# Performance work log

Measured on AMD Instinct MI355X. Metric: run time of the kernel, lower is better.

The kernel has to match this reference:

```python
import jax, jax.numpy as jnp
import numpy as np

B, S_BERT, L_WORD, D = 64, 512, 256, 768
REDUC, HID, TAGS, POL = 400, 100, 5, 4


def _make_positions():
    # Each word spans 1-2 consecutive subwords; 256 words * max 2 <= 512 subwords.
    rng = np.random.default_rng(0)
    lens = rng.integers(1, 3, size=(B, L_WORD))          # [B, L] in {1,2}
    starts = np.cumsum(lens, axis=1) - lens              # exclusive prefix sum
    ends = starts + lens - 1                             # inclusive end, <= 511
    return jnp.asarray(np.stack([starts, ends], axis=-1), dtype=jnp.int32)


def setup_inputs() -> dict:
    key = jax.random.key(0)
    ks = jax.random.split(key, 8)
    s = 0.02
    return {
        "bert_vectors": jax.random.normal(ks[0], (B, S_BERT, D), jnp.float32),
        "positions": _make_positions(),
        "W_reduc": jax.random.normal(ks[1], (D, REDUC), jnp.float32) * s,
        "b_reduc": jnp.zeros((REDUC,), jnp.float32),
        "W_ap": jax.random.normal(ks[2], (REDUC, HID), jnp.float32) * s,
        "b_ap": jnp.zeros((HID,), jnp.float32),
        "W_op": jax.random.normal(ks[3], (REDUC, HID), jnp.float32) * s,
        "b_op": jnp.zeros((HID,), jnp.float32),
        "W_ap_tag": jax.random.normal(ks[4], (HID, TAGS), jnp.float32) * s,
        "b_ap_tag": jnp.zeros((TAGS,), jnp.float32),
        "W_op_tag": jax.random.normal(ks[5], (HID, TAGS), jnp.float32) * s,
        "b_op_tag": jnp.zeros((TAGS,), jnp.float32),
        # Biaffine: bias=(True, False) -> in1 gets a ones column: [HID+1, POL*HID]
        "W_bi": jax.random.normal(ks[6], (HID + 1, POL * HID), jnp.float32) * s,
    }


def _segment_mean(vectors, positions):
    # vectors: [B, S, D]; positions: [B, L, 2] inclusive (start, end) spans.
    cs = jnp.cumsum(vectors, axis=1)
    cs = jnp.concatenate([jnp.zeros_like(cs[:, :1]), cs], axis=1)   # [B, S+1, D]
    starts = positions[..., 0]
    ends = positions[..., 1]
    hi = jnp.take_along_axis(cs, (ends + 1)[..., None], axis=1)     # [B, L, D]
    lo = jnp.take_along_axis(cs, starts[..., None], axis=1)
    lens = (ends - starts + 1).astype(vectors.dtype)[..., None]
    return (hi - lo) / lens                                          # [B, L, D]


def reference(bert_vectors, positions, W_reduc, b_reduc, W_ap, b_ap, W_op, b_op,
              W_ap_tag, b_ap_tag, W_op_tag, b_op_tag, W_bi):
    pooled = _segment_mean(bert_vectors, positions)                  # [B, L, D]
    h = jax.nn.relu(pooled @ W_reduc + b_reduc)                      # [B, L, 400]
    ap = jax.nn.relu(h @ W_ap + b_ap)                                # [B, L, 100]
    op = jax.nn.relu(h @ W_op + b_op)                                # [B, L, 100]
    ap_out = ap @ W_ap_tag + b_ap_tag                                # [B, L, T]
    op_out = op @ W_op_tag + b_op_tag                                # [B, L, T]
    # Biaffine with bias=(True, False)
    ones = jnp.ones_like(ap[..., :1])
    a1 = jnp.concatenate([ap, ones], axis=-1)                        # [B, L, 101]
    affine = (a1 @ W_bi).reshape(ap.shape[0], ap.shape[1], POL, HID) # [B, L1, P, H]
    triplet = jnp.einsum('biph,bjh->bjip', affine, op)               # [B, L2, L1, P]
    return ap_out, op_out, triplet
```

## Files before the change

### kernel.cpp

```cpp
#include <hip/hip_runtime.h>
#include <hip/hip_bf16.h>

#define B_    64
#define S_    512
#define L_    256
#define D_    768
#define RED_  400
#define REDP_ 512
#define KEFF_ 416
#define HID_  100
#define HIDP_ 128
#define TAGS_ 5
#define POL_  4
#define NBI_  512
#define NAO_  256
#define BL_   (B_ * L_)

typedef __attribute__((ext_vector_type(8))) short short8;
typedef __attribute__((ext_vector_type(4))) float f32x4;
typedef __attribute__((ext_vector_type(4))) unsigned short u16x4;

#define GLOAD_LDS16(gp, lp) __builtin_amdgcn_global_load_lds( \
    (const __attribute__((address_space(1))) void*)(gp),      \
    (__attribute__((address_space(3))) void*)(lp), 16, 0, 0)

__device__ inline float bf2f(unsigned short u) {
    union { unsigned int i; float f; } c; c.i = ((unsigned)u) << 16; return c.f;
}
__device__ inline unsigned short f2bf(float f) {
    __hip_bfloat16 h = __float2bfloat16(f);
    unsigned short u;
    __builtin_memcpy(&u, &h, 2);
    return u;
}

#define SZ0 393216
#define SZ1 131072
#define SZ2 65536
#define SZ3 512
#define SZ4 256
#define PREP_TOT (SZ0 + SZ1 + SZ2 + SZ3 + SZ4)
#define SEG_BLOCKS (BL_ / 4)
#define PREP_BLOCKS ((PREP_TOT + 255) / 256)

__global__ __launch_bounds__(256) void front_kernel(
    const float* __restrict__ bert, const int* __restrict__ pos,
    unsigned short* __restrict__ pooled,
    const float* __restrict__ W_reduc, const float* __restrict__ b_reduc,
    const float* __restrict__ W_ap, const float* __restrict__ b_ap,
    const float* __restrict__ W_op, const float* __restrict__ b_op,
    const float* __restrict__ W_bi,
    unsigned short* __restrict__ WtR, unsigned short* __restrict__ WtAO,
    unsigned short* __restrict__ WtBi,
    float* __restrict__ bR, float* __restrict__ bAO, float* __restrict__ bBi)
{
    if (blockIdx.x < SEG_BLOCKS) {
        int r  = threadIdx.x >> 6;
        int l  = threadIdx.x & 63;
        int bl = blockIdx.x * 4 + r;
        int b  = bl >> 8;
        int s  = pos[bl * 2 + 0];
        int e  = pos[bl * 2 + 1];
        int len = e - s + 1;
        const float* v0 = bert + ((size_t)b * S_ + s) * D_;
        float inv = (len == 2) ? 0.5f : 1.0f;
        unsigned short* outp = pooled + (size_t)bl * D_;
        #pragma unroll
        for (int c = 0; c < 3; ++c) {
            int d = l * 4 + c * 256;
            f32x4 x = *(const f32x4*)(v0 + d);
            if (len == 2) {
                f32x4 y = *(const f32x4*)(v0 + D_ + d);
                x += y;
            }
            u16x4 o;
            #pragma unroll
            for (int j = 0; j < 4; ++j) o[j] = f2bf(x[j] * inv);
            *(u16x4*)(outp + d) = o;
        }
        return;
    }

    int idx = (blockIdx.x - SEG_BLOCKS) * 256 + threadIdx.x;
    if (idx < SZ0) {
        int n = idx / D_, k = idx - n * D_;
        float v = (n < RED_) ? W_reduc[(size_t)k * RED_ + n] : 0.f;
        WtR[idx] = f2bf(v);
    } else if (idx < SZ0 + SZ1) {
        int i = idx - SZ0;
        int n = i >> 9, k = i & 511;
        float v = 0.f;
        if (k < RED_) {
            if (n < HID_)                      v = W_ap[(size_t)k * HID_ + n];
            else if (n >= 128 && n < 128+HID_) v = W_op[(size_t)k * HID_ + (n-128)];
        }
        WtAO[i] = f2bf(v);
    } else if (idx < SZ0 + SZ1 + SZ2) {
        int i = idx - SZ0 - SZ1;
        int n = i >> 7, k = i & 127;
        int p = n >> 7, h = n & 127;
        float v = (h < HID_ && k < HID_) ? W_bi[(size_t)k * RED_ + p * HID_ + h] : 0.f;
        WtBi[i] = f2bf(v);
        if (k == 0) bBi[n] = (h < HID_) ? W_bi[(size_t)HID_ * RED_ + p * HID_ + h] : 0.f;
    } else if (idx < SZ0 + SZ1 + SZ2 + SZ3) {
        int n = idx - SZ0 - SZ1 - SZ2;
        bR[n] = (n < RED_) ? b_reduc[n] : 0.f;
    } else if (idx < PREP_TOT) {
        int n = idx - SZ0 - SZ1 - SZ2 - SZ3;
        bAO[n] = (n < 128) ? ((n < HID_) ? b_ap[n] : 0.f)
                           : (((n-128) < HID_) ? b_op[n-128] : 0.f);
    }
}

__global__ __launch_bounds__(256) void gemm1_kernel(
    const short* __restrict__ A, const short* __restrict__ Bt,
    const float* __restrict__ bias, unsigned short* __restrict__ Co,
    int M, int N, int K)
{
    __shared__ __align__(16) short lds[2][8192];

    const int t  = threadIdx.x;
    const int wv = t >> 6;
    const int ln = t & 63;
    const int wm = wv >> 1;
    const int wn = wv & 1;
    const int bm = blockIdx.x * 128;
    const int bn = blockIdx.y * 128;

    const int srow = t >> 2;
    const int skc  = (t & 3) * 8;

    f32x4 acc[4][4] = {};
    const int NT = K >> 5;

    {
        #pragma unroll
        for (int q = 0; q < 2; ++q) {
            const short* g = A + (size_t)(bm + q * 64 + srow) * K + skc;
            GLOAD_LDS16(g, &lds[0][q * 2048 + wv * 512]);
        }
        #pragma unroll
        for (int q = 0; q < 2; ++q) {
            const short* g = Bt + (size_t)(bn + q * 64 + srow) * K + skc;
            GLOAD_LDS16(g, &lds[0][4096 + q * 2048 + wv * 512]);
        }
    }
    __syncthreads();

    int cur = 0;
    const int lr = ln & 15;
    const int lk = (ln >> 4) * 8;

    for (int kt = 0; kt < NT; ++kt) {
        if (kt + 1 < NT) {
            int k0 = (kt + 1) << 5;
            #pragma unroll
            for (int q = 0; q < 2; ++q) {
                const short* g = A + (size_t)(bm + q * 64 + srow) * K + k0 + skc;
                GLOAD_LDS16(g, &lds[cur ^ 1][q * 2048 + wv * 512]);
            }
            #pragma unroll
            for (int q = 0; q < 2; ++q) {
                const short* g = Bt + (size_t)(bn + q * 64 + srow) * K + k0 + skc;
                GLOAD_LDS16(g, &lds[cur ^ 1][4096 + q * 2048 + wv * 512]);
            }
        }

        const short* As = &lds[cur][0];
        const short* Bs = &lds[cur][4096];
        short8 a[4], b[4];
        #pragma unroll
        for (int fi = 0; fi < 4; ++fi)
            a[fi] = *(const short8*)(As + (wm * 64 + fi * 16 + lr) * 32 + lk);
        #pragma unroll
        for (int fj = 0; fj < 4; ++fj)
            b[fj] = *(const short8*)(Bs + (wn * 64 + fj * 16 + lr) * 32 + lk);
        #pragma unroll
        for (int fi = 0; fi < 4; ++fi)
            #pragma unroll
            for (int fj = 0; fj < 4; ++fj)
                acc[fi][fj] = __builtin_amdgcn_mfma_f32_16x16x32_bf16(
                    a[fi], b[fj], acc[fi][fj], 0, 0, 0);

        __syncthreads();
        cur ^= 1;
    }

    const int row0 = bm + wm * 64 + (ln >> 4) * 4;
    const int col0 = bn + wn * 64 + lr;
    #pragma unroll
    for (int fi = 0; fi < 4; ++fi)
        #pragma unroll
        for (int r = 0; r < 4; ++r) {
            int row = row0 + fi * 16 + r;
            #pragma unroll
            for (int fj = 0; fj < 4; ++fj) {
                int col = col0 + fj * 16;
                float v = fmaxf(acc[fi][fj][r] + bias[col], 0.f);
                Co[(size_t)row * N + col] = f2bf(v);
            }
        }
}

__global__ __launch_bounds__(256) void gemm23_tag_kernel(
    const short* __restrict__ A, const short* __restrict__ Bt,
    const float* __restrict__ bias,
    unsigned short* __restrict__ apOut, unsigned short* __restrict__ opOut,
    const float* __restrict__ Wap_tag, const float* __restrict__ bap_tag,
    const float* __restrict__ Wop_tag, const float* __restrict__ bop_tag,
    float* __restrict__ out_tag)
{
    __shared__ __align__(16) short lds[2][8192];
    __shared__ float tagf[128 * 101];
    __shared__ float Wtag[HID_ * TAGS_];
    __shared__ float Btag[TAGS_];

    const int t  = threadIdx.x;
    const int wv = t >> 6;
    const int ln = t & 63;
    const int wm = wv >> 1;
    const int wn = wv & 1;
    const int bm = blockIdx.x * 128;
    const int bn = blockIdx.y * 128;
    const int half = blockIdx.y;

    const float* Wt = half ? Wop_tag : Wap_tag;
    const float* bt = half ? bop_tag : bap_tag;
    for (int i = t; i < HID_ * TAGS_; i += 256) Wtag[i] = Wt[i];
    if (t < TAGS_) Btag[t] = bt[t];

    const int srow = t >> 2;
    const int skc  = (t & 3) * 8;
    const int NT = KEFF_ >> 5;

    f32x4 acc[4][4] = {};

    {
        #pragma unroll
        for (int q = 0; q < 2; ++q) {
            const short* g = A + (size_t)(bm + q * 64 + srow) * REDP_ + skc;
            GLOAD_LDS16(g, &lds[0][q * 2048 + wv * 512]);
        }
        #pragma unroll
        for (int q = 0; q < 2; ++q) {
            const short* g = Bt + (size_t)(bn + q * 64 + srow) * REDP_ + skc;
            GLOAD_LDS16(g, &lds[0][4096 + q * 2048 + wv * 512]);
        }
    }
    __syncthreads();

    int cur = 0;
    const int lr = ln & 15;
    const int lk = (ln >> 4) * 8;

    for (int kt = 0; kt < NT; ++kt) {
        if (kt + 1 < NT) {
            int k0 = (kt + 1) << 5;
            #pragma unroll
            for (int q = 0; q < 2; ++q) {
                const short* g = A + (size_t)(bm + q * 64 + srow) * REDP_ + k0 + skc;
                GLOAD_LDS16(g, &lds[cur ^ 1][q * 2048 + wv * 512]);
            }
            #pragma unroll
            for (int q = 0; q < 2; ++q) {
                const short* g = Bt + (size_t)(bn + q * 64 + srow) * REDP_ + k0 + skc;
                GLOAD_LDS16(g, &lds[cur ^ 1][4096 + q * 2048 + wv * 512]);
            }
        }

        const short* As = &lds[cur][0];
        const short* Bs = &lds[cur][4096];
        short8 a[4], b[4];
        #pragma unroll
        for (int fi = 0; fi < 4; ++fi)
            a[fi] = *(const short8*)(As + (wm * 64 + fi * 16 + lr) * 32 + lk);
        #pragma unroll
        for (int fj = 0; fj < 4; ++fj)
            b[fj] = *(const short8*)(Bs + (wn * 64 + fj * 16 + lr) * 32 + lk);
        #pragma unroll
        for (int fi = 0; fi < 4; ++fi)
            #pragma unroll
            for (int fj = 0; fj < 4; ++fj)
                acc[fi][fj] = __builtin_amdgcn_mfma_f32_16x16x32_bf16(
                    a[fi], b[fj], acc[fi][fj], 0, 0, 0);

        __syncthreads();
        cur ^= 1;
    }

    unsigned short* Co = half ? opOut : apOut;
    const int rl0 = wm * 64 + (ln >> 4) * 4;
    const int cl0 = wn * 64 + lr;
    #pragma unroll
    for (int fi = 0; fi < 4; ++fi)
        #pragma unroll
        for (int r = 0; r < 4; ++r) {
            int rl = rl0 + fi * 16 + r;
            #pragma unroll
            for (int fj = 0; fj < 4; ++fj) {
                int cl = cl0 + fj * 16;
                float v = fmaxf(acc[fi][fj][r] + bias[bn + cl], 0.f);
                Co[(size_t)(bm + rl) * 128 + cl] = f2bf(v);
                if (cl < 101) tagf[rl * 101 + cl] = v;
            }
        }
    __syncthreads();

    if (t < 128) {
        float s[TAGS_];
        #pragma unroll
        for (int g = 0; g < TAGS_; ++g) s[g] = Btag[g];
        const float* rowp = &tagf[t * 101];
        for (int k = 0; k < HID_; ++k) {
            float x = rowp[k];
            #pragma unroll
            for (int g = 0; g < TAGS_; ++g) s[g] += x * Wtag[k * TAGS_ + g];
        }
        float* o = out_tag + (size_t)half * (BL_ * TAGS_) + (size_t)(bm + t) * TAGS_;
        #pragma unroll
        for (int g = 0; g < TAGS_; ++g) o[g] = s[g];
    }
}

__global__ __launch_bounds__(256) void affine_kernel(
    const short* __restrict__ ap, const short* __restrict__ WtBi,
    const float* __restrict__ bBi, unsigned short* __restrict__ affine)
{
    __shared__ __align__(16) short As[16384];
    __shared__ __align__(16) short Bs[16384];

    const int t  = threadIdx.x;
    const int wv = t >> 6;
    const int ln = t & 63;
    const int wm = wv >> 1;
    const int wn = wv & 1;
    const int bm = blockIdx.x * 128;
    const int bn = blockIdx.y * 128;

    const int rsub = ln >> 2;
    const int j8   = (ln & 3) * 8;

    #pragma unroll
    for (int i = 0; i < 8; ++i) {
        int ks = i >> 1, hf = i & 1;
        int rloc = wv * 32 + hf * 16;
        const short* gA = ap + (size_t)(bm + rloc + rsub) * HIDP_ + ks * 32 + j8;
        GLOAD_LDS16(gA, &As[ks * 4096 + rloc * 32]);
        const short* gB = WtBi + (size_t)(bn + rloc + rsub) * HIDP_ + ks * 32 + j8;
        GLOAD_LDS16(gB, &Bs[ks * 4096 + rloc * 32]);
    }
    __syncthreads();

    const int lr = ln & 15;
    const int lk = (ln >> 4) * 8;
    f32x4 acc[4][4] = {};

    #pragma unroll
    for (int ks = 0; ks < 4; ++ks) {
        short8 a[4], b[4];
        #pragma unroll
        for (int fi = 0; fi < 4; ++fi)
            a[fi] = *(const short8*)(As + ks * 4096 + (wm * 64 + fi * 16 + lr) * 32 + lk);
        #pragma unroll
        for (int fj = 0; fj < 4; ++fj)
            b[fj] = *(const short8*)(Bs + ks * 4096 + (wn * 64 + fj * 16 + lr) * 32 + lk);
        #pragma unroll
        for (int fi = 0; fi < 4; ++fi)
            #pragma unroll
            for (int fj = 0; fj < 4; ++fj)
                acc[fi][fj] = __builtin_amdgcn_mfma_f32_16x16x32_bf16(
                    a[fi], b[fj], acc[fi][fj], 0, 0, 0);
    }

    const int row0 = bm + wm * 64 + (ln >> 4) * 4;
    const int col0 = bn + wn * 64 + lr;
    #pragma unroll
    for (int fi = 0; fi < 4; ++fi)
        #pragma unroll
        for (int r = 0; r < 4; ++r) {
            int row = row0 + fi * 16 + r;
            #pragma unroll
            for (int fj = 0; fj < 4; ++fj) {
                int col = col0 + fj * 16;
                affine[(size_t)row * NBI_ + col] = f2bf(acc[fi][fj][r] + bBi[col]);
            }
        }
}

__global__ __launch_bounds__(256) void triplet_kernel(
    const short* __restrict__ op, const short* __restrict__ affine,
    float* __restrict__ out)
{
    __shared__ __align__(16) short As[16384];
    __shared__ __align__(16) short Bs[16384];

    const int t  = threadIdx.x;
    const int wv = t >> 6;
    const int ln = t & 63;
    const int wm = wv >> 1;
    const int wn = wv & 1;
    const int bm = blockIdx.x * 128;
    const int bn = blockIdx.y * 128;
    const int b  = blockIdx.z;

    const short* Ab = op     + (size_t)b * 256 * HIDP_;
    const short* Bb = affine + (size_t)b * 256 * NBI_;

    const int rsub = ln >> 2;
    const int j8   = (ln & 3) * 8;

    #pragma unroll
    for (int i = 0; i < 8; ++i) {
        int ks = i >> 1, hf = i & 1;
        int rloc = wv * 32 + hf * 16;
        const short* gA = Ab + (size_t)(bm + rloc + rsub) * HIDP_ + ks * 32 + j8;
        GLOAD_LDS16(gA, &As[ks * 4096 + rloc * 32]);
        int ip = bn + rloc + rsub;
        const short* gB = Bb + (size_t)(ip >> 2) * NBI_ + (ip & 3) * HIDP_ + ks * 32 + j8;
        GLOAD_LDS16(gB, &Bs[ks * 4096 + rloc * 32]);
    }
    __syncthreads();

    const int lr = ln & 15;
    const int lk = (ln >> 4) * 8;
    f32x4 acc[4][4] = {};

    #pragma unroll
    for (int ks = 0; ks < 4; ++ks) {
        short8 a[4], bf[4];
        #pragma unroll
        for (int fi = 0; fi < 4; ++fi)
            a[fi] = *(const short8*)(As + ks * 4096 + (wm * 64 + fi * 16 + lr) * 32 + lk);
        #pragma unroll
        for (int fj = 0; fj < 4; ++fj)
            bf[fj] = *(const short8*)(Bs + ks * 4096 + (wn * 64 + fj * 16 + lr) * 32 + lk);
        #pragma unroll
        for (int fi = 0; fi < 4; ++fi)
            #pragma unroll
            for (int fj = 0; fj < 4; ++fj)
                acc[fi][fj] = __builtin_amdgcn_mfma_f32_16x16x32_bf16(
                    a[fi], bf[fj], acc[fi][fj], 0, 0, 0);
    }

    float* O = out + (size_t)b * 256 * 1024;
    const int row0 = bm + wm * 64 + (ln >> 4) * 4;
    const int col0 = bn + wn * 64 + lr;
    #pragma unroll
    for (int fi = 0; fi < 4; ++fi)
        #pragma unroll
        for (int r = 0; r < 4; ++r) {
            int row = row0 + fi * 16 + r;
            #pragma unroll
            for (int fj = 0; fj < 4; ++fj)
                O[(size_t)row * 1024 + col0 + fj * 16] = acc[fi][fj][r];
        }
}

extern "C" void kernel_launch(void* const* d_in, const int* in_sizes, int n_in,
                              void* d_out, int out_size, void* d_ws, size_t ws_size,
                              hipStream_t stream)
{
    const float* bert     = (const float*)d_in[0];
    const int*   pos      = (const int*)  d_in[1];
    const float* W_reduc  = (const float*)d_in[2];
    const float* b_reduc  = (const float*)d_in[3];
    const float* W_ap     = (const float*)d_in[4];
    const float* b_ap     = (const float*)d_in[5];
    const float* W_op     = (const float*)d_in[6];
    const float* b_op     = (const float*)d_in[7];
    const float* W_ap_tag = (const float*)d_in[8];
    const float* b_ap_tag = (const float*)d_in[9];
    const float* W_op_tag = (const float*)d_in[10];
    const float* b_op_tag = (const float*)d_in[11];
    const float* W_bi     = (const float*)d_in[12];

    float* out = (float*)d_out;

    char* ws = (char*)d_ws;
    unsigned short* pooled = (unsigned short*)ws; ws += (size_t)BL_ * D_ * 2;
    unsigned short* h      = (unsigned short*)ws; ws += (size_t)BL_ * REDP_ * 2;
    unsigned short* ap     = (unsigned short*)ws; ws += (size_t)BL_ * HIDP_ * 2;
    unsigned short* opv    = (unsigned short*)ws; ws += (size_t)BL_ * HIDP_ * 2;
    unsigned short* affine = (unsigned short*)ws; ws += (size_t)BL_ * NBI_ * 2;
    unsigned short* WtR    = (unsigned short*)ws; ws += (size_t)REDP_ * D_ * 2;
    unsigned short* WtAO   = (unsigned short*)ws; ws += (size_t)NAO_ * REDP_ * 2;
    unsigned short* WtBi   = (unsigned short*)ws; ws += (size_t)NBI_ * HIDP_ * 2;
    float* bR  = (float*)ws;  ws += REDP_ * 4;
    float* bAO = (float*)ws;  ws += NAO_ * 4;
    float* bBi = (float*)ws;  ws += NBI_ * 4;

    front_kernel<<<SEG_BLOCKS + PREP_BLOCKS, 256, 0, stream>>>(
        bert, pos, pooled,
        W_reduc, b_reduc, W_ap, b_ap, W_op, b_op, W_bi,
        WtR, WtAO, WtBi, bR, bAO, bBi);

    gemm1_kernel<<<dim3(BL_ / 128, REDP_ / 128), 256, 0, stream>>>(
        (const short*)pooled, (const short*)WtR, bR, h, BL_, REDP_, D_);

    gemm23_tag_kernel<<<dim3(BL_ / 128, 2), 256, 0, stream>>>(
        (const short*)h, (const short*)WtAO, bAO, ap, opv,
        W_ap_tag, b_ap_tag, W_op_tag, b_op_tag, out);

    affine_kernel<<<dim3(BL_ / 128, NBI_ / 128), 256, 0, stream>>>(
        (const short*)ap, (const short*)WtBi, bBi, affine);

    triplet_kernel<<<dim3(2, 8, B_), 256, 0, stream>>>(
        (const short*)opv, (const short*)affine, out + 2 * BL_ * TAGS_);
}
```

Baseline: 82.71 us.

## Fuse segment-mean pooling into first GEMM A-tile loads, widen N tile

Removes the separate pooled bf16 buffer by gathering the two bert subword rows for each word directly inside the first GEMM, averaging them and converting to bf16 before writing into LDS. The N tile is widened to 256 so each block covers half the output columns, which halves how many times the fp32 bert rows are re-read. The aim is to cut the pooled write and read round trip through HBM. The cost is register-staged A loads that are not asynchronous, more accumulators per thread (32 fragments), and lower occupancy.

```diff
diff --git a/kernel.cpp b/kernel.cpp
--- a/kernel.cpp
+++ b/kernel.cpp
@@ -40,12 +40,9 @@
 #define SZ3 512
 #define SZ4 256
 #define PREP_TOT (SZ0 + SZ1 + SZ2 + SZ3 + SZ4)
-#define SEG_BLOCKS (BL_ / 4)
 #define PREP_BLOCKS ((PREP_TOT + 255) / 256)
 
-__global__ __launch_bounds__(256) void front_kernel(
-    const float* __restrict__ bert, const int* __restrict__ pos,
-    unsigned short* __restrict__ pooled,
+__global__ __launch_bounds__(256) void prep_kernel(
     const float* __restrict__ W_reduc, const float* __restrict__ b_reduc,
     const float* __restrict__ W_ap, const float* __restrict__ b_ap,
     const float* __restrict__ W_op, const float* __restrict__ b_op,
@@ -54,34 +51,7 @@
     unsigned short* __restrict__ WtBi,
     float* __restrict__ bR, float* __restrict__ bAO, float* __restrict__ bBi)
 {
-    if (blockIdx.x < SEG_BLOCKS) {
-        int r  = threadIdx.x >> 6;
-        int l  = threadIdx.x & 63;
-        int bl = blockIdx.x * 4 + r;
-        int b  = bl >> 8;
-        int s  = pos[bl * 2 + 0];
-        int e  = pos[bl * 2 + 1];
-        int len = e - s + 1;
-        const float* v0 = bert + ((size_t)b * S_ + s) * D_;
-        float inv = (len == 2) ? 0.5f : 1.0f;
-        unsigned short* outp = pooled + (size_t)bl * D_;
-        #pragma unroll
-        for (int c = 0; c < 3; ++c) {
-            int d = l * 4 + c * 256;
-            f32x4 x = *(const f32x4*)(v0 + d);
-            if (len == 2) {
-                f32x4 y = *(const f32x4*)(v0 + D_ + d);
-                x += y;
-            }
-            u16x4 o;
-            #pragma unroll
-            for (int j = 0; j < 4; ++j) o[j] = f2bf(x[j] * inv);
-            *(u16x4*)(outp + d) = o;
-        }
-        return;
-    }
-
-    int idx = (blockIdx.x - SEG_BLOCKS) * 256 + threadIdx.x;
+    int idx = blockIdx.x * 256 + threadIdx.x;
     if (idx < SZ0) {
         int n = idx / D_, k = idx - n * D_;
         float v = (n < RED_) ? W_reduc[(size_t)k * RED_ + n] : 0.f;
@@ -112,37 +82,56 @@
     }
 }
 
-__global__ __launch_bounds__(256) void gemm1_kernel(
-    const short* __restrict__ A, const short* __restrict__ Bt,
-    const float* __restrict__ bias, unsigned short* __restrict__ Co,
-    int M, int N, int K)
+__global__ __launch_bounds__(256) void gemm1_seg_kernel(
+    const float* __restrict__ bert, const int* __restrict__ pos,
+    const short* __restrict__ Bt, const float* __restrict__ bias,
+    unsigned short* __restrict__ Co)
 {
-    __shared__ __align__(16) short lds[2][8192];
+    __shared__ __align__(16) short lds[2][12288];
 
     const int t  = threadIdx.x;
     const int wv = t >> 6;
     const int ln = t & 63;
     const int wm = wv >> 1;
     const int wn = wv & 1;
-    const int bm = blockIdx.x * 128;
-    const int bn = blockIdx.y * 128;
+    const int bm  = blockIdx.x * 128;
+    const int bnh = blockIdx.y * 256;
+    const int batch = bm >> 8;
 
     const int srow = t >> 2;
     const int skc  = (t & 3) * 8;
 
-    f32x4 acc[4][4] = {};
-    const int NT = K >> 5;
+    size_t rb0[2], rb1[2];
+    #pragma unroll
+    for (int q = 0; q < 2; ++q) {
+        int r = bm + q * 64 + srow;
+        int s = pos[r * 2 + 0];
+        int e = pos[r * 2 + 1];
+        rb0[q] = ((size_t)batch * S_ + s) * D_;
+        rb1[q] = ((size_t)batch * S_ + e) * D_;
+    }
+
+    f32x4 acc[4][8] = {};
+    const int NT = D_ >> 5;
 
     {
         #pragma unroll
+        for (int q = 0; q < 4; ++q) {
+            const short* g = Bt + (size_t)(bnh + q * 64 + srow) * D_ + skc;
+            GLOAD_LDS16(g, &lds[0][4096 + q * 2048 + wv * 512]);
+        }
+        #pragma unroll
         for (int q = 0; q < 2; ++q) {
-            const short* g = A + (size_t)(bm + q * 64 + srow) * K + skc;
-            GLOAD_LDS16(g, &lds[0][q * 2048 + wv * 512]);
-        }
-        #pragma unroll
-        for (int q = 0; q < 2; ++q) {
-            const short* g = Bt + (size_t)(bn + q * 64 + srow) * K + skc;
-            GLOAD_LDS16(g, &lds[0][4096 + q * 2048 + wv * 512]);
+            f32x4 x0 = *(const f32x4*)(bert + rb0[q] + skc);
+            f32x4 x1 = *(const f32x4*)(bert + rb0[q] + skc + 4);
+            f32x4 y0 = *(const f32x4*)(bert + rb1[q] + skc);
+            f32x4 y1 = *(const f32x4*)(bert + rb1[q] + skc + 4);
+            f32x4 s0 = (x0 + y0) * 0.5f;
+            f32x4 s1 = (x1 + y1) * 0.5f;
+            union { short8 v; unsigned short u[8]; } o;
+            #pragma unroll
+            for (int j = 0; j < 4; ++j) { o.u[j] = f2bf(s0[j]); o.u[4+j] = f2bf(s1[j]); }
+            *(short8*)(&lds[0][(q * 64 + srow) * 32 + skc]) = o.v;
         }
     }
     __syncthreads();
@@ -152,52 +141,68 @@
     const int lk = (ln >> 4) * 8;
 
     for (int kt = 0; kt < NT; ++kt) {
-        if (kt + 1 < NT) {
-            int k0 = (kt + 1) << 5;
+        const bool more = (kt + 1 < NT);
+        f32x4 x0[2], x1[2], y0[2], y1[2];
+        if (more) {
+            int col = (kt + 1) * 32 + skc;
             #pragma unroll
             for (int q = 0; q < 2; ++q) {
-                const short* g = A + (size_t)(bm + q * 64 + srow) * K + k0 + skc;
-                GLOAD_LDS16(g, &lds[cur ^ 1][q * 2048 + wv * 512]);
-            }
-            #pragma unroll
-            for (int q = 0; q < 2; ++q) {
-                const short* g = Bt + (size_t)(bn + q * 64 + srow) * K + k0 + skc;
+                x0[q] = *(const f32x4*)(bert + rb0[q] + col);
+                x1[q] = *(const f32x4*)(bert + rb0[q] + col + 4);
+                y0[q] = *(const f32x4*)(bert + rb1[q] + col);
+                y1[q] = *(const f32x4*)(bert + rb1[q] + col + 4);
+            }
+            #pragma unroll
+            for (int q = 0; q < 4; ++q) {
+                const short* g = Bt + (size_t)(bnh + q * 64 + srow) * D_ + (kt + 1) * 32 + skc;
                 GLOAD_LDS16(g, &lds[cur ^ 1][4096 + q * 2048 + wv * 512]);
             }
         }
 
         const short* As = &lds[cur][0];
         const short* Bs = &lds[cur][4096];
-        short8 a[4], b[4];
+        short8 a[4], b[8];
         #pragma unroll
         for (int fi = 0; fi < 4; ++fi)
             a[fi] = *(const short8*)(As + (wm * 64 + fi * 16 + lr) * 32 + lk);
         #pragma unroll
-        for (int fj = 0; fj < 4; ++fj)
-            b[fj] = *(const short8*)(Bs + (wn * 64 + fj * 16 + lr) * 32 + lk);
-        #pragma unroll
-        for (int fi = 0; fi < 4; ++fi)
-            #pragma unroll
-            for (int fj = 0; fj < 4; ++fj)
+        for (int fj = 0; fj < 8; ++fj)
+            b[fj] = *(const short8*)(Bs + (wn * 128 + fj * 16 + lr) * 32 + lk);
+        #pragma unroll
+        for (int fi = 0; fi < 4; ++fi)
+            #pragma unroll
+            for (int fj = 0; fj < 8; ++fj)
                 acc[fi][fj] = __builtin_amdgcn_mfma_f32_16x16x32_bf16(
                     a[fi], b[fj], acc[fi][fj], 0, 0, 0);
 
+        if (more) {
+            #pragma unroll
+            for (int q = 0; q < 2; ++q) {
+                f32x4 s0 = (x0[q] + y0[q]) * 0.5f;
+                f32x4 s1 = (x1[q] + y1[q]) * 0.5f;
+                union { short8 v; unsigned short u[8]; } o;
+                #pragma unroll
+                for (int j = 0; j < 4; ++j) { o.u[j] = f2bf(s0[j]); o.u[4+j] = f2bf(s1[j]); }
+                *(short8*)(&lds[cur ^ 1][(q * 64 + srow) * 32 + skc]) = o.v;
+            }
+        }
+
         __syncthreads();
         cur ^= 1;
     }
 
     const int row0 = bm + wm * 64 + (ln >> 4) * 4;
-    const int col0 = bn + wn * 64 + lr;
+    const int col0 = bnh + wn * 128 + lr;
     #pragma unroll
     for (int fi = 0; fi < 4; ++fi)
         #pragma unroll
         for (int r = 0; r < 4; ++r) {
             int row = row0 + fi * 16 + r;
             #pragma unroll
-            for (int fj = 0; fj < 4; ++fj) {
+            for (int fj = 0; fj < 8; ++fj) {
                 int col = col0 + fj * 16;
                 float v = fmaxf(acc[fi][fj][r] + bias[col], 0.f);
-                Co[(size_t)row * N + col] = f2bf(v);
+                Co[(size_t)row * REDP_ + col] = f2bf(v);
             }
         }
 }
@@ -477,7 +482,6 @@
     float* out = (float*)d_out;
 
     char* ws = (char*)d_ws;
-    unsigned short* pooled = (unsigned short*)ws; ws += (size_t)BL_ * D_ * 2;
     unsigned short* h      = (unsigned short*)ws; ws += (size_t)BL_ * REDP_ * 2;
     unsigned short* ap     = (unsigned short*)ws; ws += (size_t)BL_ * HIDP_ * 2;
     unsigned short* opv    = (unsigned short*)ws; ws += (size_t)BL_ * HIDP_ * 2;
@@ -489,13 +493,12 @@
     float* bAO = (float*)ws;  ws += NAO_ * 4;
     float* bBi = (float*)ws;  ws += NBI_ * 4;
 
-    front_kernel<<<SEG_BLOCKS + PREP_BLOCKS, 256, 0, stream>>>(
-        bert, pos, pooled,
+    prep_kernel<<<PREP_BLOCKS, 256, 0, stream>>>(
         W_reduc, b_reduc, W_ap, b_ap, W_op, b_op, W_bi,
         WtR, WtAO, WtBi, bR, bAO, bBi);
 
-    gemm1_kernel<<<dim3(BL_ / 128, REDP_ / 128), 256, 0, stream>>>(
-        (const short*)pooled, (const short*)WtR, bR, h, BL_, REDP_, D_);
+    gemm1_seg_kernel<<<dim3(BL_ / 128, 2), 256, 0, stream>>>(
+        bert, pos, (const short*)WtR, bR, h);
 
     gemm23_tag_kernel<<<dim3(BL_ / 128, 2), 256, 0, stream>>>(
         (const short*)h, (const short*)WtAO, bAO, ap, opv,
```

Measured after the change: 85.03 us. +2.8%, slower.
